# Optimization experiments

Hardware: AMD Instinct MI355X
Metric: run time of the kernel (lower is better)

The kernel has to match this reference:

```python
import jax, jax.numpy as jnp
import numpy as np

SCALE = 8.0  # sqrt(head_dim=64); module divides scores by self.scale


def setup_inputs() -> dict:
    key = jax.random.key(0)
    kq, kk, kv = jax.random.split(key, 3)
    B, H, L, D = 4, 8, 2048, 64
    queries = jax.random.normal(kq, (B, H, L, D), dtype=jnp.float32)
    keys = jax.random.normal(kk, (B, H, L, D), dtype=jnp.float32)
    values = jax.random.normal(kv, (B, H, L, D), dtype=jnp.float32)
    return {"queries": queries, "keys": keys, "values": values}


def reference(queries, keys, values):
    # scores: [B, H, L_Q, L_K]
    L_Q, L_K = queries.shape[2], keys.shape[2]
    scores = jnp.einsum('bnqd,bnkd->bnqk', queries, keys) / SCALE
    # causal mask: triu(ones, diagonal=1) positions set to -inf
    causal = jnp.triu(jnp.ones((L_Q, L_K), dtype=bool), k=1)
    scores = jnp.where(causal[None, None, :, :], -jnp.inf, scores)
    A = jax.nn.softmax(scores, axis=-1)  # dropout p=0.0 (eval) -> identity
    V = jnp.einsum('bnqk,bnkd->bnqd', A, values)
    return V
```

## Files before the change

### kernel.cpp

```cpp
#include <hip/hip_runtime.h>
#include <hip/hip_bf16.h>

typedef __attribute__((ext_vector_type(8))) short bf16x8;
typedef __attribute__((ext_vector_type(16))) float f32x16;

#define DHEAD 64
#define L_SEQ 2048
#define QSCALE (0.125f * 1.44269504088896340736f)

#define WS_ML_OFF   4096
#define WS_PART_OFF (4096 + 512 * 2 * 128 * 8)
#define WS_NEED     ((size_t)WS_PART_OFF + (size_t)512 * 128 * 64 * 2)

union U4S8 { uint4 u; bf16x8 s; };

__device__ __forceinline__ unsigned pk2(float a, float b) {
    unsigned r;
    asm("v_cvt_pk_bf16_f32 %0, %1, %2" : "=v"(r) : "v"(a), "v"(b));
    return r;
}
__device__ __forceinline__ float bfrt(float x) {
    return __uint_as_float(pk2(x, x) << 16);
}
__device__ __forceinline__ float bf2f(unsigned short u) {
    return __uint_as_float((unsigned)u << 16);
}

__device__ __forceinline__ float fexp2(float x) {
#if __has_builtin(__builtin_amdgcn_exp2f)
    return __builtin_amdgcn_exp2f(x);
#else
    return __expf(x * 0.69314718055994530942f);
#endif
}

#define MAX16(P) fmaxf(fmaxf(fmaxf(fmaxf(P[0],P[1]),fmaxf(P[2],P[3])),          \
                             fmaxf(fmaxf(P[4],P[5]),fmaxf(P[6],P[7]))),         \
                       fmaxf(fmaxf(fmaxf(P[8],P[9]),fmaxf(P[10],P[11])),        \
                             fmaxf(fmaxf(P[12],P[13]),fmaxf(P[14],P[15]))))
#define SUM16(P) ((((P[0]+P[1])+(P[2]+P[3]))+((P[4]+P[5])+(P[6]+P[7])))         \
                + (((P[8]+P[9])+(P[10]+P[11]))+((P[12]+P[13])+(P[14]+P[15]))))


template<int SPLIT>
__global__ __launch_bounds__(256, 3)
void fattn_kernel(const float* __restrict__ Qg, const float* __restrict__ Kg,
                  const float* __restrict__ Vg, float* __restrict__ Og,
                  char* __restrict__ wsBase) {
    __shared__ uint4 sK4[16][64];
    __shared__ uint4 sV4[16][64];

    const int tid  = threadIdx.x;
    const int lane = tid & 63;
    const int w    = tid >> 6;
    const int hi   = lane >> 5;
    const int c    = lane & 31;

    const int id  = blockIdx.x;
    const int bh  = (id & 7) + 8 * ((id >> 3) & 3);

    int T, h, kt0, kstep, d;
    if (SPLIT) {
        const int k31 = 31 - (id >> 5);
        T = k31 >> 1;
        h = 1 - (k31 & 1);
        d = (T + 2 - h) >> 1;
        if (d == 0) return;
        kt0 = h; kstep = 2;
    } else {
        const int u_ = id >> 5;
        T = (u_ < 8) ? (15 - u_) : (u_ - 8);
        h = 0; d = T + 1; kt0 = 0; kstep = 1;
    }

    const size_t base = (size_t)bh * L_SEQ * DHEAD;
    const int q0w = T * 128 + w * 32;

    bf16x8 qf[4];
    {
        const float* Qrow = Qg + base + (size_t)(q0w + c) * DHEAD;
        #pragma unroll
        for (int kc = 0; kc < 4; ++kc) {
            float4 aa = *(const float4*)(Qrow + kc * 16 + hi * 8);
            float4 bb = *(const float4*)(Qrow + kc * 16 + hi * 8 + 4);
            U4S8 t;
            t.u = make_uint4(pk2(aa.x * QSCALE, aa.y * QSCALE),
                             pk2(aa.z * QSCALE, aa.w * QSCALE),
                             pk2(bb.x * QSCALE, bb.y * QSCALE),
                             pk2(bb.z * QSCALE, bb.w * QSCALE));
            qf[kc] = t.s;
        }
    }

    const float* Kpb = Kg + base + (size_t)(32 * w + c) * DHEAD + 32 * hi;
    const float* Vpb = Vg + base + (size_t)(32 * w + 16 * hi) * DHEAD + c;

    auto stage_K = [&](int kt) {
        float4 rk[8];
        const float* Kp = Kpb + (size_t)kt * 128 * DHEAD;
        #pragma unroll
        for (int t = 0; t < 8; ++t) rk[t] = *(const float4*)(Kp + 4 * t);
        #pragma unroll
        for (int q = 0; q < 2; ++q)
            #pragma unroll
            for (int hh = 0; hh < 2; ++hh) {
                const float4 r0 = rk[4 * q + 2 * hh], r1 = rk[4 * q + 2 * hh + 1];
                sK4[w * 4 + 2 * hi + q][hh * 32 + c] =
                    make_uint4(pk2(r0.x, r0.y), pk2(r0.z, r0.w),
                               pk2(r1.x, r1.y), pk2(r1.z, r1.w));
            }
    };
    auto stage_V = [&](int kt) {
        float rv[32];
        const float* Vp = Vpb + (size_t)kt * 128 * DHEAD;
        #pragma unroll
        for (int j = 0; j < 16; ++j) {
            rv[j]      = Vp[j * DHEAD];
            rv[16 + j] = Vp[j * DHEAD + 32];
        }
        #pragma unroll
        for (int dt = 0; dt < 2; ++dt)
            #pragma unroll
            for (int hh = 0; hh < 2; ++hh) {
                const int b = 16 * dt + 8 * hh;
                sV4[(2 * w + hi) * 2 + dt][hh * 32 + c] =
                    make_uint4(pk2(rv[b + 0], rv[b + 1]), pk2(rv[b + 2], rv[b + 3]),
                               pk2(rv[b + 4], rv[b + 5]), pk2(rv[b + 6], rv[b + 7]));
            }
    };

    f32x16 o0 = {0,0,0,0,0,0,0,0,0,0,0,0,0,0,0,0};
    f32x16 o1 = o0;
    float m_r = -1e30f, l_r = 0.f;

    stage_K(kt0);
    stage_V(kt0);
    __syncthreads();

    for (int j = 0; j < d; ++j) {
        const int  kt   = kt0 + j * kstep;
        const bool pf   = (j + 1 < d);
        const bool diag = (kt == T);

        #pragma unroll
        for (int sub = 0; sub < 2; ++sub) {
            const int lim = diag ? (w + 1 - 2 * sub) : 2;
            const int nkb = lim < 0 ? 0 : (lim > 2 ? 2 : lim);
            if (nkb > 0) {
                float p[2][16];

                __builtin_amdgcn_s_setprio(1);
                #pragma unroll
                for (int i = 0; i < 2; ++i) {
                    if (i < nkb) {
                        f32x16 s = {0,0,0,0,0,0,0,0,0,0,0,0,0,0,0,0};
                        #pragma unroll
                        for (int kc = 0; kc < 4; ++kc) {
                            U4S8 t; t.u = sK4[(2 * sub + i) * 4 + kc][lane];
                            s = __builtin_amdgcn_mfma_f32_32x32x16_bf16(t.s, qf[kc], s, 0, 0, 0);
                        }
                        #pragma unroll
                        for (int r = 0; r < 16; ++r) p[i][r] = s[r];
                    }
                }
                __builtin_amdgcn_s_setprio(0);

                #pragma unroll
                for (int i = 0; i < 2; ++i) {
                    if (diag && (2 * sub + i) == w) {
                        #pragma unroll
                        for (int r = 0; r < 16; ++r) {
                            const int kk = (r & 3) + 8 * (r >> 2) + 4 * hi;
                            if (kk > c) p[i][r] = -1e30f;
                        }
                    }
                }

                float mx = MAX16(p[0]);
                if (nkb > 1) mx = fmaxf(mx, MAX16(p[1]));
                mx = fmaxf(mx, __shfl_xor(mx, 32));

                if (__any(mx > m_r + 8.f)) {
                    const float mn    = fmaxf(m_r, mx);
                    const float alpha = fexp2(m_r - mn);
                    m_r  = mn;
                    l_r *= alpha;
                    #pragma unroll
                    for (int r = 0; r < 16; ++r) {
                        const float ab = __shfl(alpha, (r & 3) + 8 * (r >> 2) + 4 * hi);
                        o0[r] *= ab; o1[r] *= ab;
                    }
                }

                #pragma unroll
                for (int i = 0; i < 2; ++i) {
                    if (i < nkb) {
                        #pragma unroll
                        for (int r = 0; r < 16; ++r) p[i][r] = fexp2(p[i][r] - m_r);
                    }
                }
                float rs = SUM16(p[0]);
                if (nkb > 1) rs += SUM16(p[1]);
                rs += __shfl_xor(rs, 32);
                l_r += rs;

                __builtin_amdgcn_s_setprio(1);
                #pragma unroll
                for (int kcl = 0; kcl < 4; ++kcl) {
                    if (kcl < 2 * nkb) {
                        const int i = kcl >> 1, bs = (kcl & 1) * 8;
                        unsigned a0 = pk2(p[i][bs + 0], p[i][bs + 1]);
                        unsigned a1 = pk2(p[i][bs + 2], p[i][bs + 3]);
                        unsigned b0 = pk2(p[i][bs + 4], p[i][bs + 5]);
                        unsigned b1 = pk2(p[i][bs + 6], p[i][bs + 7]);
                        asm("v_permlane32_swap_b32 %0, %1" : "+v"(a0), "+v"(b0));
                        asm("v_permlane32_swap_b32 %0, %1" : "+v"(a1), "+v"(b1));
                        U4S8 t;
                        t.u = make_uint4(a0, a1, b0, b1);
                        const int kv = 4 * sub + kcl;
                        U4S8 tv0; tv0.u = sV4[kv * 2][lane];
                        o0 = __builtin_amdgcn_mfma_f32_32x32x16_bf16(t.s, tv0.s, o0, 0, 0, 0);
                        U4S8 tv1; tv1.u = sV4[kv * 2 + 1][lane];
                        o1 = __builtin_amdgcn_mfma_f32_32x32x16_bf16(t.s, tv1.s, o1, 0, 0, 0);
                    }
                }
                __builtin_amdgcn_s_setprio(0);
            }
        }

        if (pf) {
            __syncthreads();
            stage_K(kt + kstep);
            stage_V(kt + kstep);
            __syncthreads();
        }
    }

    float* Op = Og + base;

    if (!SPLIT || T == 0) {
        const float linv = 1.f / l_r;
        #pragma unroll
        for (int r = 0; r < 16; ++r) {
            const int   cr  = (r & 3) + 8 * (r >> 2) + 4 * hi;
            const float lb  = __shfl(linv, cr);
            const int   row = q0w + cr;
            Op[(size_t)row * DHEAD + c]      = o0[r] * lb;
            Op[(size_t)row * DHEAD + 32 + c] = o1[r] * lb;
        }
        return;
    }

    const int f = bh * 16 + T;
    float2* ml = (float2*)(wsBase + WS_ML_OFF);
    if (hi == 0) ml[((size_t)f * 2 + h) * 128 + w * 32 + c] = make_float2(m_r, l_r);
    if (h == 0) {
        #pragma unroll
        for (int r = 0; r < 16; ++r) {
            const int cr  = (r & 3) + 8 * (r >> 2) + 4 * hi;
            const int row = q0w + cr;
            Op[(size_t)row * DHEAD + c]      = bfrt(o0[r]);
            Op[(size_t)row * DHEAD + 32 + c] = bfrt(o1[r]);
        }
    } else {
        unsigned short* mp = (unsigned short*)(wsBase + WS_PART_OFF) + (size_t)f * 128 * 64;
        #pragma unroll
        for (int r = 0; r < 16; ++r) {
            const int cr   = (r & 3) + 8 * (r >> 2) + 4 * hi;
            const int lrow = w * 32 + cr;
            mp[lrow * 64 + c]      = (unsigned short)pk2(o0[r], o0[r]);
            mp[lrow * 64 + 32 + c] = (unsigned short)pk2(o1[r], o1[r]);
        }
    }
}

__global__ __launch_bounds__(256)
void merge_kernel(float* __restrict__ Og, const char* __restrict__ wsBase) {
    const int blk = blockIdx.x;
    const int bh = blk >> 4, T = blk & 15;
    if (T == 0) return;
    const int f = bh * 16 + T;

    const float2* ml = (const float2*)(wsBase + WS_ML_OFF);
    const unsigned short* part =
        (const unsigned short*)(wsBase + WS_PART_OFF) + (size_t)f * 128 * 64;
    float* Op = Og + ((size_t)bh * L_SEQ + (size_t)T * 128) * DHEAD;

    __shared__ float sA0[128], sA1[128], sLi[128];
    const int t = threadIdx.x;
    if (t < 128) {
        const float2 m0 = ml[((size_t)f * 2 + 0) * 128 + t];
        const float2 m1 = ml[((size_t)f * 2 + 1) * 128 + t];
        const float mM = fmaxf(m0.x, m1.x);
        const float a0 = fexp2(m0.x - mM);
        const float a1 = fexp2(m1.x - mM);
        sA0[t] = a0; sA1[t] = a1;
        sLi[t] = 1.f / (a0 * m0.y + a1 * m1.y);
    }
    __syncthreads();

    #pragma unroll
    for (int e = 0; e < 8; ++e) {
        const int idx4 = e * 256 + t;
        const int row  = idx4 >> 4;
        const int c4   = (idx4 & 15) * 4;
        const float a0 = sA0[row], a1 = sA1[row], li = sLi[row];
        float4 po = *(float4*)&Op[row * 64 + c4];
        const ushort4 u = *(const ushort4*)&part[row * 64 + c4];
        po.x = (a0 * po.x + a1 * bf2f(u.x)) * li;
        po.y = (a0 * po.y + a1 * bf2f(u.y)) * li;
        po.z = (a0 * po.z + a1 * bf2f(u.z)) * li;
        po.w = (a0 * po.w + a1 * bf2f(u.w)) * li;
        *(float4*)&Op[row * 64 + c4] = po;
    }
}

extern "C" void kernel_launch(void* const* d_in, const int* in_sizes, int n_in,
                              void* d_out, int out_size, void* d_ws, size_t ws_size,
                              hipStream_t stream) {
    const float* Q = (const float*)d_in[0];
    const float* K = (const float*)d_in[1];
    const float* V = (const float*)d_in[2];
    float* O = (float*)d_out;
    if (ws_size >= WS_NEED) {
        fattn_kernel<1><<<dim3(1024), dim3(256), 0, stream>>>(Q, K, V, O, (char*)d_ws);
        merge_kernel<<<dim3(512), dim3(256), 0, stream>>>(O, (const char*)d_ws);
    } else {
        fattn_kernel<0><<<dim3(512), dim3(256), 0, stream>>>(Q, K, V, O, (char*)d_ws);
    }
}
```

Before: 52.13 us.

## Split causal KV range into contiguous 4-tile chunks with job table scheduling

```diff
diff --git a/kernel.cpp b/kernel.cpp
--- a/kernel.cpp
+++ b/kernel.cpp
@@ -9,8 +9,8 @@
 #define QSCALE (0.125f * 1.44269504088896340736f)
 
 #define WS_ML_OFF   4096
-#define WS_PART_OFF (4096 + 512 * 2 * 128 * 8)
-#define WS_NEED     ((size_t)WS_PART_OFF + (size_t)512 * 128 * 64 * 2)
+#define WS_PART_OFF (4096 + 2048 * 128 * 8)
+#define WS_NEED     ((size_t)WS_PART_OFF + (size_t)768 * 128 * 64 * 2)
 
 union U4S8 { uint4 u; bf16x8 s; };
 
@@ -41,8 +41,24 @@
 #define SUM16(P) ((((P[0]+P[1])+(P[2]+P[3]))+((P[4]+P[5])+(P[6]+P[7])))         \
                 + (((P[8]+P[9])+(P[10]+P[11]))+((P[12]+P[13])+(P[14]+P[15]))))
 
-
-template<int SPLIT>
+__constant__ unsigned char JOBS[40] = {
+    (15<<2)|0, (15<<2)|1, (15<<2)|2, (15<<2)|3,
+    (14<<2)|0, (14<<2)|1, (14<<2)|2,
+    (13<<2)|0, (13<<2)|1, (13<<2)|2,
+    (12<<2)|0, (12<<2)|1, (12<<2)|2,
+    (11<<2)|0, (11<<2)|1, (11<<2)|2,
+    (10<<2)|0, (10<<2)|1,
+    ( 9<<2)|0, ( 9<<2)|1,
+    ( 8<<2)|0, ( 8<<2)|1,
+    ( 7<<2)|0, ( 7<<2)|1,
+    ( 6<<2)|0, ( 5<<2)|0, ( 4<<2)|0, ( 3<<2)|0,
+    (14<<2)|3, (10<<2)|2, ( 6<<2)|1, ( 2<<2)|0,
+    (13<<2)|3, ( 9<<2)|2, ( 5<<2)|1, ( 1<<2)|0,
+    (12<<2)|3, ( 8<<2)|2, ( 4<<2)|1, ( 0<<2)|0,
+};
+
+
+template<int MODE>
 __global__ __launch_bounds__(256, 3)
 void fattn_kernel(const float* __restrict__ Qg, const float* __restrict__ Kg,
                   const float* __restrict__ Vg, float* __restrict__ Og,
@@ -59,18 +75,17 @@
     const int id  = blockIdx.x;
     const int bh  = (id & 7) + 8 * ((id >> 3) & 3);
 
-    int T, h, kt0, kstep, d;
-    if (SPLIT) {
-        const int k31 = 31 - (id >> 5);
-        T = k31 >> 1;
-        h = 1 - (k31 & 1);
-        d = (T + 2 - h) >> 1;
-        if (d == 0) return;
-        kt0 = h; kstep = 2;
+    int T, sg, kt0, d;
+    if (MODE == 2) {
+        const unsigned jb = JOBS[id >> 5];
+        T   = jb >> 2;
+        sg  = jb & 3;
+        kt0 = 4 * sg;
+        d   = T - kt0 + 1; if (d > 4) d = 4;
     } else {
         const int u_ = id >> 5;
         T = (u_ < 8) ? (15 - u_) : (u_ - 8);
-        h = 0; d = T + 1; kt0 = 0; kstep = 1;
+        sg = 0; kt0 = 0; d = T + 1;
     }
 
     const size_t base = (size_t)bh * L_SEQ * DHEAD;
@@ -138,7 +153,7 @@
     __syncthreads();
 
     for (int j = 0; j < d; ++j) {
-        const int  kt   = kt0 + j * kstep;
+        const int  kt   = kt0 + j;
         const bool pf   = (j + 1 < d);
         const bool diag = (kt == T);
 
@@ -230,15 +245,15 @@
 
         if (pf) {
             __syncthreads();
-            stage_K(kt + kstep);
-            stage_V(kt + kstep);
+            stage_K(kt + 1);
+            stage_V(kt + 1);
             __syncthreads();
         }
     }
 
     float* Op = Og + base;
 
-    if (!SPLIT || T == 0) {
+    if (MODE == 0 || T <= 3) {
         const float linv = 1.f / l_r;
         #pragma unroll
         for (int r = 0; r < 16; ++r) {
@@ -251,10 +266,10 @@
         return;
     }
 
-    const int f = bh * 16 + T;
+    const int f4 = (bh * 16 + T) * 4;
     float2* ml = (float2*)(wsBase + WS_ML_OFF);
-    if (hi == 0) ml[((size_t)f * 2 + h) * 128 + w * 32 + c] = make_float2(m_r, l_r);
-    if (h == 0) {
+    if (hi == 0) ml[(size_t)(f4 + sg) * 128 + w * 32 + c] = make_float2(m_r, l_r);
+    if (sg == 0) {
         #pragma unroll
         for (int r = 0; r < 16; ++r) {
             const int cr  = (r & 3) + 8 * (r >> 2) + 4 * hi;
@@ -263,7 +278,9 @@
             Op[(size_t)row * DHEAD + 32 + c] = bfrt(o1[r]);
         }
     } else {
-        unsigned short* mp = (unsigned short*)(wsBase + WS_PART_OFF) + (size_t)f * 128 * 64;
+        const int g  = T >> 2;
+        const int ps = bh * 24 + 2 * g * (g - 1) + (T & 3) * g + (sg - 1);
+        unsigned short* mp = (unsigned short*)(wsBase + WS_PART_OFF) + (size_t)ps * 128 * 64;
         #pragma unroll
         for (int r = 0; r < 16; ++r) {
             const int cr   = (r & 3) + 8 * (r >> 2) + 4 * hi;
@@ -278,24 +295,31 @@
 void merge_kernel(float* __restrict__ Og, const char* __restrict__ wsBase) {
     const int blk = blockIdx.x;
     const int bh = blk >> 4, T = blk & 15;
-    if (T == 0) return;
-    const int f = bh * 16 + T;
+    if (T <= 3) return;
+    const int n  = (T >> 2) + 1;
+    const int f4 = (bh * 16 + T) * 4;
+    const int g  = T >> 2;
+    const int psb = bh * 24 + 2 * g * (g - 1) + (T & 3) * g;
 
     const float2* ml = (const float2*)(wsBase + WS_ML_OFF);
-    const unsigned short* part =
-        (const unsigned short*)(wsBase + WS_PART_OFF) + (size_t)f * 128 * 64;
+    const unsigned short* part = (const unsigned short*)(wsBase + WS_PART_OFF);
+    const unsigned short* p1 = part + (size_t)(psb + 0) * 128 * 64;
+    const unsigned short* p2 = part + (size_t)(psb + 1) * 128 * 64;
+    const unsigned short* p3 = part + (size_t)(psb + 2) * 128 * 64;
     float* Op = Og + ((size_t)bh * L_SEQ + (size_t)T * 128) * DHEAD;
 
-    __shared__ float sA0[128], sA1[128], sLi[128];
+    __shared__ float sA0[128], sA1[128], sA2[128], sA3[128], sLi[128];
     const int t = threadIdx.x;
     if (t < 128) {
-        const float2 m0 = ml[((size_t)f * 2 + 0) * 128 + t];
-        const float2 m1 = ml[((size_t)f * 2 + 1) * 128 + t];
-        const float mM = fmaxf(m0.x, m1.x);
-        const float a0 = fexp2(m0.x - mM);
-        const float a1 = fexp2(m1.x - mM);
-        sA0[t] = a0; sA1[t] = a1;
-        sLi[t] = 1.f / (a0 * m0.y + a1 * m1.y);
+        const float2 m0 = ml[(size_t)(f4 + 0) * 128 + t];
+        const float2 m1 = ml[(size_t)(f4 + 1) * 128 + t];
+        const float2 m2 = (n > 2) ? ml[(size_t)(f4 + 2) * 128 + t] : make_float2(-1e30f, 0.f);
+        const float2 m3 = (n > 3) ? ml[(size_t)(f4 + 3) * 128 + t] : make_float2(-1e30f, 0.f);
+        const float mM = fmaxf(fmaxf(m0.x, m1.x), fmaxf(m2.x, m3.x));
+        const float a0 = fexp2(m0.x - mM), a1 = fexp2(m1.x - mM);
+        const float a2 = fexp2(m2.x - mM), a3 = fexp2(m3.x - mM);
+        sA0[t] = a0; sA1[t] = a1; sA2[t] = a2; sA3[t] = a3;
+        sLi[t] = 1.f / (a0 * m0.y + a1 * m1.y + a2 * m2.y + a3 * m3.y);
     }
     __syncthreads();
 
@@ -304,14 +328,30 @@
         const int idx4 = e * 256 + t;
         const int row  = idx4 >> 4;
         const int c4   = (idx4 & 15) * 4;
-        const float a0 = sA0[row], a1 = sA1[row], li = sLi[row];
-        float4 po = *(float4*)&Op[row * 64 + c4];
-        const ushort4 u = *(const ushort4*)&part[row * 64 + c4];
-        po.x = (a0 * po.x + a1 * bf2f(u.x)) * li;
-        po.y = (a0 * po.y + a1 * bf2f(u.y)) * li;
-        po.z = (a0 * po.z + a1 * bf2f(u.z)) * li;
-        po.w = (a0 * po.w + a1 * bf2f(u.w)) * li;
-        *(float4*)&Op[row * 64 + c4] = po;
+        const int off  = row * 64 + c4;
+        const float a0 = sA0[row], li = sLi[row];
+        float4 po = *(float4*)&Op[off];
+        po.x *= a0; po.y *= a0; po.z *= a0; po.w *= a0;
+        {
+            const float a1 = sA1[row];
+            const ushort4 u = *(const ushort4*)&p1[off];
+            po.x += a1 * bf2f(u.x); po.y += a1 * bf2f(u.y);
+            po.z += a1 * bf2f(u.z); po.w += a1 * bf2f(u.w);
+        }
+        if (n > 2) {
+            const float a2 = sA2[row];
+            const ushort4 u = *(const ushort4*)&p2[off];
+            po.x += a2 * bf2f(u.x); po.y += a2 * bf2f(u.y);
+            po.z += a2 * bf2f(u.z); po.w += a2 * bf2f(u.w);
+        }
+        if (n > 3) {
+            const float a3 = sA3[row];
+            const ushort4 u = *(const ushort4*)&p3[off];
+            po.x += a3 * bf2f(u.x); po.y += a3 * bf2f(u.y);
+            po.z += a3 * bf2f(u.z); po.w += a3 * bf2f(u.w);
+        }
+        po.x *= li; po.y *= li; po.z *= li; po.w *= li;
+        *(float4*)&Op[off] = po;
     }
 }
 
@@ -323,7 +363,7 @@
     const float* V = (const float*)d_in[2];
     float* O = (float*)d_out;
     if (ws_size >= WS_NEED) {
-        fattn_kernel<1><<<dim3(1024), dim3(256), 0, stream>>>(Q, K, V, O, (char*)d_ws);
+        fattn_kernel<2><<<dim3(1280), dim3(256), 0, stream>>>(Q, K, V, O, (char*)d_ws);
         merge_kernel<<<dim3(512), dim3(256), 0, stream>>>(O, (const char*)d_ws);
     } else {
         fattn_kernel<0><<<dim3(512), dim3(256), 0, stream>>>(Q, K, V, O, (char*)d_ws);
```

Measured after the change: 64.24 us. +23.2%, slower.
